# Kernel optimization log

Measured on AMD Instinct MI355X. Metric: run time of the kernel, lower is better.

## Reference

```python
import jax, jax.numpy as jnp
import numpy as np

D = 2048      # d_model
FF = 8192     # d_ff
S = 4096      # seq_len == max_len
EPS = 1.1920929e-07  # torch.finfo(float32).eps (nn.RMSNorm default when eps=None)
SCALE = float(np.sqrt(D))


def _rms_norm(x, w):
    # x: [S, D]
    return x * jax.lax.rsqrt(jnp.mean(x * x, axis=-1, keepdims=True) + EPS) * w


def _rope(x, cos, sin):
    # x: [S, D]; cos/sin: [S, D/2]
    x1, x2 = jnp.split(x, 2, axis=-1)
    return jnp.concatenate([x1 * cos - x2 * sin, x1 * sin + x2 * cos], axis=-1)


def setup_inputs() -> dict:
    key = jax.random.key(0)
    ks = jax.random.split(key, 9)

    def w(k, shape, scale=0.02):
        return jax.random.normal(k, shape, dtype=jnp.float32) * scale

    x = jax.random.normal(ks[0], (S, D), dtype=jnp.float32)
    # torch nn.Linear stores weight as [out, in]; forward is x @ W.T
    wq = w(ks[1], (D, D))
    wk = w(ks[2], (D, D))
    wv = w(ks[3], (D, D))
    wo = w(ks[4], (D, D))
    w_gate = w(ks[5], (FF, D))
    w_up = w(ks[6], (FF, D))
    w_down = w(ks[7], (D, FF))
    w_rn1 = jnp.ones((D,), dtype=jnp.float32)
    w_rn2 = jnp.ones((D,), dtype=jnp.float32)
    # RoPE caches (buffers)
    freqs = 1.0 / 10000.0 ** (jnp.arange(0, D, 2, dtype=jnp.float32) / D)
    t = jnp.arange(S, dtype=jnp.float32)
    angles = jnp.outer(t, freqs)  # [S, D/2]
    cos = jnp.cos(angles)
    sin = jnp.sin(angles)
    return dict(x=x, w_rn1=w_rn1, wq=wq, wk=wk, wv=wv, wo=wo,
                w_rn2=w_rn2, w_gate=w_gate, w_up=w_up, w_down=w_down,
                cos=cos, sin=sin)


def reference(x, w_rn1, wq, wk, wv, wo, w_rn2, w_gate, w_up, w_down, cos, sin):
    h = _rms_norm(x, w_rn1)                      # [S, D]
    q = _rope(h @ wq.T, cos, sin)                # [S, D]
    k = _rope(h @ wk.T, cos, sin)                # [S, D]
    v = h @ wv.T                                 # [S, D]
    attn = jax.nn.softmax(q @ k.T / SCALE, axis=-1)  # [S, S]
    x = x + (attn @ v) @ wo.T                    # residual 1
    h = _rms_norm(x, w_rn2)
    ffn = (jax.nn.silu(h @ w_gate.T) * (h @ w_up.T)) @ w_down.T  # SwiGLU
    return x + ffn
```

## Files before the change

### kernel.cpp

```cpp
#include <hip/hip_runtime.h>

#define S_LEN 4096
#define D_MODEL 2048
#define FF_DIM 8192
#define QKV_LD 6144

typedef __attribute__((ext_vector_type(8))) short s16x8;
typedef __attribute__((ext_vector_type(4))) short s16x4;
typedef __attribute__((ext_vector_type(4))) float f32x4;

__device__ __forceinline__ short f2bf(float f) {
  union { float f; unsigned u; } c; c.f = f;
  unsigned r = (c.u + 0x7fffu + ((c.u >> 16) & 1u)) >> 16;
  return (short)r;
}
__device__ __forceinline__ float bf2f(short s) {
  union { unsigned u; float f; } c; c.u = ((unsigned)(unsigned short)s) << 16;
  return c.f;
}

#define GLDS16(g, l) __builtin_amdgcn_global_load_lds( \
    (const __attribute__((address_space(1))) unsigned*)(g), \
    (__attribute__((address_space(3))) unsigned*)(l), 16, 0, 0)

__device__ __forceinline__ int swz(int b) {
  return b ^ (((b >> 7) & 7) << 4);
}

#define BAR()   __builtin_amdgcn_s_barrier()
#define LGKM0() asm volatile("s_waitcnt lgkmcnt(0)" ::: "memory")
#define VMC(n)  asm volatile("s_waitcnt vmcnt(" #n ")" ::: "memory")

__global__ void conv_f32_bf16(const float* __restrict__ in, short* __restrict__ out, long n) {
  long i = ((long)blockIdx.x * blockDim.x + threadIdx.x) * 8;
  if (i >= n) return;
  f32x4 a = *(const f32x4*)(in + i);
  f32x4 b = *(const f32x4*)(in + i + 4);
  s16x8 o;
  o[0] = f2bf(a[0]); o[1] = f2bf(a[1]); o[2] = f2bf(a[2]); o[3] = f2bf(a[3]);
  o[4] = f2bf(b[0]); o[5] = f2bf(b[1]); o[6] = f2bf(b[2]); o[7] = f2bf(b[3]);
  *(s16x8*)(out + i) = o;
}

__global__ void rmsnorm_kernel(const float* __restrict__ x, const float* __restrict__ w,
                               short* __restrict__ out) {
  const int row = blockIdx.x;
  const int t = threadIdx.x;
  const float* xr = x + (long)row * D_MODEL;
  f32x4 v0 = ((const f32x4*)xr)[t];
  f32x4 v1 = ((const f32x4*)xr)[256 + t];
  float ss = v0[0]*v0[0] + v0[1]*v0[1] + v0[2]*v0[2] + v0[3]*v0[3]
           + v1[0]*v1[0] + v1[1]*v1[1] + v1[2]*v1[2] + v1[3]*v1[3];
  #pragma unroll
  for (int o = 32; o > 0; o >>= 1) ss += __shfl_xor(ss, o, 64);
  __shared__ float red[4];
  if ((t & 63) == 0) red[t >> 6] = ss;
  __syncthreads();
  ss = red[0] + red[1] + red[2] + red[3];
  float scale = rsqrtf(ss * (1.0f / D_MODEL) + 1.1920929e-07f);
  f32x4 w0 = ((const f32x4*)w)[t];
  f32x4 w1 = ((const f32x4*)w)[256 + t];
  s16x4 o0, o1;
  #pragma unroll
  for (int i = 0; i < 4; i++) {
    o0[i] = f2bf(v0[i] * scale * w0[i]);
    o1[i] = f2bf(v1[i] * scale * w1[i]);
  }
  short* orow = out + (long)row * D_MODEL;
  ((s16x4*)orow)[t] = o0;
  ((s16x4*)orow)[256 + t] = o1;
}

__global__ void rope_kernel(short* __restrict__ qkv,
                            const float* __restrict__ cosb, const float* __restrict__ sinb) {
  const int s = blockIdx.x;
  short* row = qkv + (long)s * QKV_LD + (blockIdx.y ? D_MODEL : 0);
  const int j = threadIdx.x * 4;
  f32x4 c = *(const f32x4*)(cosb + (long)s * (D_MODEL / 2) + j);
  f32x4 sn = *(const f32x4*)(sinb + (long)s * (D_MODEL / 2) + j);
  s16x4 x1 = *(s16x4*)(row + j);
  s16x4 x2 = *(s16x4*)(row + (D_MODEL / 2) + j);
  s16x4 o1, o2;
  #pragma unroll
  for (int i = 0; i < 4; i++) {
    float a = bf2f(x1[i]), b = bf2f(x2[i]);
    o1[i] = f2bf(a * c[i] - b * sn[i]);
    o2[i] = f2bf(a * sn[i] + b * c[i]);
  }
  *(s16x4*)(row + j) = o1;
  *(s16x4*)(row + (D_MODEL / 2) + j) = o2;
}

__global__ void transpose_kernel(const short* __restrict__ in, short* __restrict__ out,
                                 int R, int C, int ld) {
  __shared__ short tile[32][33];
  const int bx = blockIdx.x * 32, by = blockIdx.y * 32;
  const int x = threadIdx.x, y = threadIdx.y;
  #pragma unroll
  for (int i = 0; i < 32; i += 8) tile[y + i][x] = in[(long)(by + y + i) * ld + bx + x];
  __syncthreads();
  #pragma unroll
  for (int i = 0; i < 32; i += 8) out[(long)(bx + y + i) * R + by + x] = tile[x][y + i];
}

__global__ void softmax_kernel(const float* __restrict__ sraw, short* __restrict__ pb) {
  const int row = blockIdx.x;
  const int t = threadIdx.x;
  const float* rp = sraw + (long)row * S_LEN;
  f32x4 v[4];
  #pragma unroll
  for (int i = 0; i < 4; i++) v[i] = ((const f32x4*)rp)[i * 256 + t];
  float m = -1e30f;
  #pragma unroll
  for (int i = 0; i < 4; i++)
    m = fmaxf(m, fmaxf(fmaxf(v[i][0], v[i][1]), fmaxf(v[i][2], v[i][3])));
  #pragma unroll
  for (int o = 32; o > 0; o >>= 1) m = fmaxf(m, __shfl_xor(m, o, 64));
  __shared__ float redm[4], reds[4];
  if ((t & 63) == 0) redm[t >> 6] = m;
  __syncthreads();
  m = fmaxf(fmaxf(redm[0], redm[1]), fmaxf(redm[2], redm[3]));
  float sum = 0.f;
  #pragma unroll
  for (int i = 0; i < 4; i++) {
    #pragma unroll
    for (int j = 0; j < 4; j++) { v[i][j] = __expf(v[i][j] - m); sum += v[i][j]; }
  }
  #pragma unroll
  for (int o = 32; o > 0; o >>= 1) sum += __shfl_xor(sum, o, 64);
  if ((t & 63) == 0) reds[t >> 6] = sum;
  __syncthreads();
  sum = reds[0] + reds[1] + reds[2] + reds[3];
  float inv = 1.0f / sum;
  short* prow = pb + (long)row * S_LEN;
  #pragma unroll
  for (int i = 0; i < 4; i++) {
    s16x4 o;
    #pragma unroll
    for (int j = 0; j < 4; j++) o[j] = f2bf(v[i][j] * inv);
    ((s16x4*)prow)[i * 256 + t] = o;
  }
}

template <int EPI>
__device__ __forceinline__ void epi_store(float v, long idx, float* Cf, short* Cb,
                                          const short* gmul, const float* res, float scale) {
  if (EPI == 0)      Cb[idx] = f2bf(v);
  else if (EPI == 1) Cb[idx] = f2bf(v / (1.0f + __expf(-v)));
  else if (EPI == 2) Cb[idx] = f2bf(bf2f(gmul[idx]) * v);
  else if (EPI == 3) Cf[idx] = v * scale;
  else               Cf[idx] = res[idx] + v;
}

template <int EPI>
__global__ __launch_bounds__(512)
void gemm8p_n256(const short* __restrict__ A, const short* __restrict__ B,
                 float* __restrict__ Cf, short* __restrict__ Cb,
                 const short* __restrict__ gmul, const float* __restrict__ res,
                 int K, int lda, int ldb, int ldc, float scale) {
  __shared__ short lds[2][32768];
  const int t = threadIdx.x;
  const int lane = t & 63, wid = t >> 6;
  const int wr = wid >> 2, wc = wid & 3;
  const int llo = lane & 15, lhi = lane >> 4;

  const int nwg = gridDim.x * gridDim.y;
  int bid = blockIdx.y * gridDim.x + blockIdx.x;
  bid = (bid & 7) * (nwg >> 3) + (bid >> 3);
  const long m0 = (long)(bid / gridDim.x) * 256;
  const long n0 = (long)(bid % gridDim.x) * 256;

  const int c0 = t, c1 = t + 512;
  const int sb0 = swz(c0 * 16), sb1 = swz(c1 * 16);
  const short* srcA0 = A + (m0 + (sb0 >> 7)) * (long)lda + ((sb0 & 127) >> 1);
  const short* srcA1 = A + (m0 + (sb1 >> 7)) * (long)lda + ((sb1 & 127) >> 1);
  const short* srcB0 = B + (n0 + (sb0 >> 7)) * (long)ldb + ((sb0 & 127) >> 1);
  const short* srcB1 = B + (n0 + (sb1 >> 7)) * (long)ldb + ((sb1 & 127) >> 1);
  const long dA = 128L * lda, dB = 128L * ldb;
  const int NT = K >> 6, NI = NT >> 1;

  int aof[4][2], bof[2][2];
  #pragma unroll
  for (int mf = 0; mf < 4; mf++)
    #pragma unroll
    for (int ks = 0; ks < 2; ks++)
      aof[mf][ks] = swz((wr * 128 + mf * 16 + llo) * 128 + ks * 64 + lhi * 16) >> 1;
  #pragma unroll
  for (int nf = 0; nf < 2; nf++)
    #pragma unroll
    for (int ks = 0; ks < 2; ks++)
      bof[nf][ks] = swz(32768 + (wc * 64 + nf * 16 + llo) * 128 + ks * 64 + lhi * 16) >> 1;

  f32x4 acc[8][4];
  #pragma unroll
  for (int m = 0; m < 8; m++)
    #pragma unroll
    for (int n = 0; n < 4; n++) acc[m][n] = (f32x4)(0.f);

  s16x8 ar[4][2], b0r[2][2], b1r[2][2];

  auto stage = [&](int tt, int p) {
    if (tt >= NT) return;
    short* dst = (short*)lds[tt & 1] + p * 8192;
    const long kk = (long)tt * 64;
    const short *s0, *s1;
    if (p == 0)      { s0 = srcA0;      s1 = srcA1; }
    else if (p == 1) { s0 = srcA0 + dA; s1 = srcA1 + dA; }
    else if (p == 2) { s0 = srcB0;      s1 = srcB1; }
    else             { s0 = srcB0 + dB; s1 = srcB1 + dB; }
    GLDS16(s0 + kk, dst + c0 * 8);
    GLDS16(s1 + kk, dst + c1 * 8);
  };

#define LDA6(BUF, MH) { const short* lp = (const short*)lds[BUF]; \
  _Pragma("unroll") for (int mf = 0; mf < 4; mf++) \
  _Pragma("unroll") for (int ks = 0; ks < 2; ks++) \
    ar[mf][ks] = *(const s16x8*)(lp + aof[mf][ks] + (MH) * 4096); }
#define LDB6(BUF, NH, DST) { const short* lp = (const short*)lds[BUF]; \
  _Pragma("unroll") for (int nf = 0; nf < 2; nf++) \
  _Pragma("unroll") for (int ks = 0; ks < 2; ks++) \
    DST[nf][ks] = *(const s16x8*)(lp + bof[nf][ks] + (NH) * 2048); }
#define MFMAQ6(MH, NH, BR) { __builtin_amdgcn_s_setprio(1); \
  _Pragma("unroll") for (int ks = 0; ks < 2; ks++) \
  _Pragma("unroll") for (int mf = 0; mf < 4; mf++) \
  _Pragma("unroll") for (int nf = 0; nf < 2; nf++) \
    acc[(MH)*4+mf][(NH)*2+nf] = __builtin_amdgcn_mfma_f32_16x16x32_bf16( \
        ar[mf][ks], BR[nf][ks], acc[(MH)*4+mf][(NH)*2+nf], 0, 0, 0); \
  __builtin_amdgcn_s_setprio(0); }

  stage(0, 0); stage(0, 1); stage(0, 2); stage(0, 3);
  stage(1, 2); stage(1, 3);
  VMC(4); BAR();

  for (int it = 0; it < NI; ++it) {
    const int tt = it * 2;
    const bool last = (it == NI - 1);
    LDA6(0, 0); LDB6(0, 0, b0r); stage(tt + 1, 0);
    BAR(); LGKM0(); MFMAQ6(0, 0, b0r); BAR();
    LDB6(0, 1, b1r); stage(tt + 1, 1);
    BAR(); LGKM0(); MFMAQ6(0, 1, b1r); BAR();
    LDA6(0, 1); stage(tt + 2, 2);
    BAR(); LGKM0(); MFMAQ6(1, 1, b1r); BAR();
    stage(tt + 2, 3);
    if (last) { VMC(0); } else { VMC(4); }
    BAR(); MFMAQ6(1, 0, b0r); BAR();
    LDA6(1, 0); LDB6(1, 0, b0r); stage(tt + 2, 0);
    BAR(); LGKM0(); MFMAQ6(0, 0, b0r); BAR();
    LDB6(1, 1, b1r); stage(tt + 2, 1);
    BAR(); LGKM0(); MFMAQ6(0, 1, b1r); BAR();
    LDA6(1, 1); stage(tt + 3, 2);
    BAR(); LGKM0(); MFMAQ6(1, 1, b1r); BAR();
    stage(tt + 3, 3);
    if (last) { VMC(0); } else { VMC(4); }
    BAR(); MFMAQ6(1, 0, b0r); BAR();
  }

  #pragma unroll
  for (int mf = 0; mf < 8; mf++) {
    const long row0 = m0 + wr * 128 + mf * 16 + lhi * 4;
    #pragma unroll
    for (int j = 0; j < 4; j++) {
      const long col = n0 + wc * 64 + (j >> 1) * 32 + (j & 1) * 16 + llo;
      #pragma unroll
      for (int r = 0; r < 4; r++)
        epi_store<EPI>(acc[mf][j][r], (row0 + r) * (long)ldc + col, Cf, Cb, gmul, res, scale);
    }
  }
#undef LDA6
#undef LDB6
#undef MFMAQ6
}

template <int EPI>
__global__ __launch_bounds__(512)
void gemm8p_n128(const short* __restrict__ A, const short* __restrict__ B,
                 float* __restrict__ Cf, short* __restrict__ Cb,
                 const short* __restrict__ gmul, const float* __restrict__ res,
                 int K, int lda, int ldb, int ldc, float scale) {
  __shared__ short lds[3][24576];
  const int t = threadIdx.x;
  const int lane = t & 63, wid = t >> 6;
  const int wr = wid >> 1, wc = wid & 1;
  const int llo = lane & 15, lhi = lane >> 4;

  const int nwg = gridDim.x * gridDim.y;
  int bid = blockIdx.y * gridDim.x + blockIdx.x;
  bid = (bid & 7) * (nwg >> 3) + (bid >> 3);
  const long m0 = (long)(bid / gridDim.x) * 256;
  const long n0 = (long)(bid % gridDim.x) * 128;

  const int c0 = t, c1 = t + 512;
  const int sb0 = swz(c0 * 16), sb1 = swz(c1 * 16);
  const short* srcA0 = A + (m0 + (sb0 >> 7)) * (long)lda + ((sb0 & 127) >> 1);
  const short* srcA1 = A + (m0 + (sb1 >> 7)) * (long)lda + ((sb1 & 127) >> 1);
  const short* srcB0 = B + (n0 + (sb0 >> 7)) * (long)ldb + ((sb0 & 127) >> 1);
  const short* srcB1 = B + (n0 + (sb1 >> 7)) * (long)ldb + ((sb1 & 127) >> 1);
  const long dA = 128L * lda;
  const int NT = K >> 6;

  int aof[4][2], bof[2][2];
  #pragma unroll
  for (int mf = 0; mf < 4; mf++)
    #pragma unroll
    for (int ks = 0; ks < 2; ks++)
      aof[mf][ks] = swz((wr * 64 + mf * 16 + llo) * 128 + ks * 64 + lhi * 16) >> 1;
  #pragma unroll
  for (int nf = 0; nf < 2; nf++)
    #pragma unroll
    for (int ks = 0; ks < 2; ks++)
      bof[nf][ks] = swz(32768 + (wc * 64 + nf * 16 + llo) * 128 + ks * 64 + lhi * 16) >> 1;

  f32x4 acc[4][4];
  #pragma unroll
  for (int m = 0; m < 4; m++)
    #pragma unroll
    for (int n = 0; n < 4; n++) acc[m][n] = (f32x4)(0.f);

  s16x8 ar[4][2], br[2][2];

  auto stage = [&](int tt, int slot, int p) {
    if (tt >= NT) return;
    short* dst = (short*)lds[slot] + p * 8192;
    const long kk = (long)tt * 64;
    const short *s0, *s1;
    if (p == 0)      { s0 = srcA0;      s1 = srcA1; }
    else if (p == 1) { s0 = srcA0 + dA; s1 = srcA1 + dA; }
    else             { s0 = srcB0;      s1 = srcB1; }
    GLDS16(s0 + kk, dst + c0 * 8);
    GLDS16(s1 + kk, dst + c1 * 8);
  };

#define LDA3(CUR) { const short* lp = (const short*)lds[CUR]; \
  _Pragma("unroll") for (int mf = 0; mf < 4; mf++) \
  _Pragma("unroll") for (int ks = 0; ks < 2; ks++) \
    ar[mf][ks] = *(const s16x8*)(lp + aof[mf][ks]); }
#define LDB3(CUR, NH) { const short* lp = (const short*)lds[CUR]; \
  _Pragma("unroll") for (int nf = 0; nf < 2; nf++) \
  _Pragma("unroll") for (int ks = 0; ks < 2; ks++) \
    br[nf][ks] = *(const s16x8*)(lp + bof[nf][ks] + (NH) * 2048); }
#define MFMAQ3(NH) { __builtin_amdgcn_s_setprio(1); \
  _Pragma("unroll") for (int ks = 0; ks < 2; ks++) \
  _Pragma("unroll") for (int mf = 0; mf < 4; mf++) \
  _Pragma("unroll") for (int nf = 0; nf < 2; nf++) \
    acc[mf][(NH)*2+nf] = __builtin_amdgcn_mfma_f32_16x16x32_bf16( \
        ar[mf][ks], br[nf][ks], acc[mf][(NH)*2+nf], 0, 0, 0); \
  __builtin_amdgcn_s_setprio(0); }

  stage(0, 0, 0); stage(0, 0, 1); stage(0, 0, 2);
  stage(1, 1, 0); stage(1, 1, 1); stage(1, 1, 2);
  VMC(6); BAR();

  int cur = 0;
  for (int tt = 0; tt < NT; ++tt) {
    const int s2 = (cur >= 1) ? cur - 1 : 2;
    LDA3(cur); LDB3(cur, 0); stage(tt + 2, s2, 0); stage(tt + 2, s2, 1);
    BAR(); LGKM0(); MFMAQ3(0); BAR();
    LDB3(cur, 1); stage(tt + 2, s2, 2);
    if (tt >= NT - 2) { VMC(0); } else { VMC(6); }
    BAR(); LGKM0(); MFMAQ3(1); BAR();
    cur = (cur == 2) ? 0 : cur + 1;
  }

  #pragma unroll
  for (int mf = 0; mf < 4; mf++) {
    const long row0 = m0 + wr * 64 + mf * 16 + lhi * 4;
    #pragma unroll
    for (int j = 0; j < 4; j++) {
      const long col = n0 + wc * 64 + (j >> 1) * 32 + (j & 1) * 16 + llo;
      #pragma unroll
      for (int r = 0; r < 4; r++)
        epi_store<EPI>(acc[mf][j][r], (row0 + r) * (long)ldc + col, Cf, Cb, gmul, res, scale);
    }
  }
#undef LDA3
#undef LDB3
#undef MFMAQ3
}

extern "C" void kernel_launch(void* const* d_in, const int* in_sizes, int n_in,
                              void* d_out, int out_size, void* d_ws, size_t ws_size,
                              hipStream_t stream) {
  const float* x      = (const float*)d_in[0];
  const float* w_rn1  = (const float*)d_in[1];
  const float* wq     = (const float*)d_in[2];
  const float* wk     = (const float*)d_in[3];
  const float* wv     = (const float*)d_in[4];
  const float* wo     = (const float*)d_in[5];
  const float* w_rn2  = (const float*)d_in[6];
  const float* w_gate = (const float*)d_in[7];
  const float* w_up   = (const float*)d_in[8];
  const float* w_down = (const float*)d_in[9];
  const float* cosb   = (const float*)d_in[10];
  const float* sinb   = (const float*)d_in[11];
  float* out = (float*)d_out;

  const long S = S_LEN, D = D_MODEL, FF = FF_DIM;
  char* ws = (char*)d_ws;
  size_t off = 0;
  auto alloc = [&](size_t bytes) { void* p = ws + off; off += (bytes + 255) & ~(size_t)255; return p; };

  short* qkv  = (short*)alloc(S * QKV_LD * 2);
  short* vT   = (short*)alloc(D * S * 2);
  short* hb   = (short*)alloc(S * D * 2);
  float* x1   = (float*)alloc(S * D * 4);
  short* wbuf = (short*)alloc(FF * D * 2);
  char*  u2   = (char*)alloc(S * S * 4);
  float* sraw = (float*)u2;
  short* gbuf = (short*)u2;
  short* pb   = (short*)alloc(S * S * 2);

  const float inv_scale = 1.0f / sqrtf((float)D_MODEL);
  const long DD = D * D, FD = FF * D;
  const int convDD = (int)(DD / 8 / 256), convFD = (int)(FD / 8 / 256);
  dim3 blk(256), blk5(512);
  dim3 gQKV(3 * D_MODEL / 256, S_LEN / 256);
  dim3 gS(S_LEN / 256, S_LEN / 256);
  dim3 gN2048(D_MODEL / 128, S_LEN / 256);
  dim3 gF(FF_DIM / 256, S_LEN / 256);

  rmsnorm_kernel<<<S_LEN, 256, 0, stream>>>(x, w_rn1, hb);
  conv_f32_bf16<<<convDD, blk, 0, stream>>>(wq, wbuf, DD);
  conv_f32_bf16<<<convDD, blk, 0, stream>>>(wk, wbuf + DD, DD);
  conv_f32_bf16<<<convDD, blk, 0, stream>>>(wv, wbuf + 2 * DD, DD);
  gemm8p_n256<0><<<gQKV, blk5, 0, stream>>>(hb, wbuf, nullptr, qkv, nullptr, nullptr,
                                            D_MODEL, D_MODEL, D_MODEL, QKV_LD, 1.f);
  rope_kernel<<<dim3(S_LEN, 2), blk, 0, stream>>>(qkv, cosb, sinb);
  transpose_kernel<<<dim3(D_MODEL / 32, S_LEN / 32), dim3(32, 8), 0, stream>>>(
      qkv + 2 * D_MODEL, vT, S_LEN, D_MODEL, QKV_LD);
  gemm8p_n256<3><<<gS, blk5, 0, stream>>>(qkv, qkv + D_MODEL, sraw, nullptr, nullptr, nullptr,
                                          D_MODEL, QKV_LD, QKV_LD, S_LEN, inv_scale);
  softmax_kernel<<<S_LEN, 256, 0, stream>>>(sraw, pb);
  gemm8p_n128<0><<<gN2048, blk5, 0, stream>>>(pb, vT, nullptr, qkv + 2 * D_MODEL, nullptr, nullptr,
                                              S_LEN, S_LEN, S_LEN, QKV_LD, 1.f);
  conv_f32_bf16<<<convDD, blk, 0, stream>>>(wo, wbuf, DD);
  gemm8p_n128<4><<<gN2048, blk5, 0, stream>>>(qkv + 2 * D_MODEL, wbuf, x1, nullptr, nullptr, x,
                                              D_MODEL, QKV_LD, D_MODEL, D_MODEL, 1.f);
  rmsnorm_kernel<<<S_LEN, 256, 0, stream>>>(x1, w_rn2, hb);
  conv_f32_bf16<<<convFD, blk, 0, stream>>>(w_gate, wbuf, FD);
  gemm8p_n256<1><<<gF, blk5, 0, stream>>>(hb, wbuf, nullptr, gbuf, nullptr, nullptr,
                                          D_MODEL, D_MODEL, D_MODEL, FF_DIM, 1.f);
  conv_f32_bf16<<<convFD, blk, 0, stream>>>(w_up, wbuf, FD);
  gemm8p_n256<2><<<gF, blk5, 0, stream>>>(hb, wbuf, nullptr, gbuf, gbuf, nullptr,
                                          D_MODEL, D_MODEL, D_MODEL, FF_DIM, 1.f);
  conv_f32_bf16<<<convFD, blk, 0, stream>>>(w_down, wbuf, FD);
  gemm8p_n128<4><<<gN2048, blk5, 0, stream>>>(gbuf, wbuf, out, nullptr, nullptr, x1,
                                              FF_DIM, FF_DIM, FF_DIM, D_MODEL, 1.f);
}
```

Before: 858.9 us.

## Restructure GEMM main loops to one barrier per K-tile with staged lgkmcnt waits

Both GEMM kernels drop the eight-phase, barrier-heavy ping-pong schedule. Each K-tile now issues all LDS fragment reads up front, then all global-to-LDS prefetches for a later tile. MFMA groups are gated by partial lgkmcnt waits, and a single barrier closes each iteration. This cuts barrier count and lets MFMAs start while the remaining LDS reads are still in flight. The trade-offs are more fragment registers live at once (a0r/a1r/b0r/b1r), and in the 256x256 kernel a wait for all outstanding global loads (vmcnt 0) every iteration, so prefetch can only overlap one tile of compute.

```diff
diff --git a/kernel.cpp b/kernel.cpp
--- a/kernel.cpp
+++ b/kernel.cpp
@@ -28,8 +28,9 @@
 }
 
 #define BAR()   __builtin_amdgcn_s_barrier()
-#define LGKM0() asm volatile("s_waitcnt lgkmcnt(0)" ::: "memory")
 #define VMC(n)  asm volatile("s_waitcnt vmcnt(" #n ")" ::: "memory")
+#define LGKM(n) asm volatile("s_waitcnt lgkmcnt(" #n ")" ::: "memory"); \
+                __builtin_amdgcn_sched_barrier(0)
 
 __global__ void conv_f32_bf16(const float* __restrict__ in, short* __restrict__ out, long n) {
   long i = ((long)blockIdx.x * blockDim.x + threadIdx.x) * 8;
@@ -177,7 +178,7 @@
   const short* srcB0 = B + (n0 + (sb0 >> 7)) * (long)ldb + ((sb0 & 127) >> 1);
   const short* srcB1 = B + (n0 + (sb1 >> 7)) * (long)ldb + ((sb1 & 127) >> 1);
   const long dA = 128L * lda, dB = 128L * ldb;
-  const int NT = K >> 6, NI = NT >> 1;
+  const int NT = K >> 6;
 
   int aof[4][2], bof[2][2];
   #pragma unroll
@@ -197,62 +198,52 @@
     #pragma unroll
     for (int n = 0; n < 4; n++) acc[m][n] = (f32x4)(0.f);
 
-  s16x8 ar[4][2], b0r[2][2], b1r[2][2];
-
-  auto stage = [&](int tt, int p) {
+  s16x8 a0r[4][2], a1r[4][2], b0r[2][2], b1r[2][2];
+
+  auto stageAll = [&](int tt) {
     if (tt >= NT) return;
-    short* dst = (short*)lds[tt & 1] + p * 8192;
+    short* dst = (short*)lds[tt & 1];
     const long kk = (long)tt * 64;
-    const short *s0, *s1;
-    if (p == 0)      { s0 = srcA0;      s1 = srcA1; }
-    else if (p == 1) { s0 = srcA0 + dA; s1 = srcA1 + dA; }
-    else if (p == 2) { s0 = srcB0;      s1 = srcB1; }
-    else             { s0 = srcB0 + dB; s1 = srcB1 + dB; }
-    GLDS16(s0 + kk, dst + c0 * 8);
-    GLDS16(s1 + kk, dst + c1 * 8);
+    GLDS16(srcA0 + kk,      dst + c0 * 8);
+    GLDS16(srcA1 + kk,      dst + c1 * 8);
+    GLDS16(srcA0 + dA + kk, dst + 8192 + c0 * 8);
+    GLDS16(srcA1 + dA + kk, dst + 8192 + c1 * 8);
+    GLDS16(srcB0 + kk,      dst + 16384 + c0 * 8);
+    GLDS16(srcB1 + kk,      dst + 16384 + c1 * 8);
+    GLDS16(srcB0 + dB + kk, dst + 24576 + c0 * 8);
+    GLDS16(srcB1 + dB + kk, dst + 24576 + c1 * 8);
   };
 
-#define LDA6(BUF, MH) { const short* lp = (const short*)lds[BUF]; \
+#define RDA6(DST, MH) { \
   _Pragma("unroll") for (int mf = 0; mf < 4; mf++) \
   _Pragma("unroll") for (int ks = 0; ks < 2; ks++) \
-    ar[mf][ks] = *(const s16x8*)(lp + aof[mf][ks] + (MH) * 4096); }
-#define LDB6(BUF, NH, DST) { const short* lp = (const short*)lds[BUF]; \
+    DST[mf][ks] = *(const s16x8*)(lp + aof[mf][ks] + (MH) * 4096); }
+#define RDB6(DST, NH) { \
   _Pragma("unroll") for (int nf = 0; nf < 2; nf++) \
   _Pragma("unroll") for (int ks = 0; ks < 2; ks++) \
     DST[nf][ks] = *(const s16x8*)(lp + bof[nf][ks] + (NH) * 2048); }
-#define MFMAQ6(MH, NH, BR) { __builtin_amdgcn_s_setprio(1); \
+#define MQ6(AR, BR, MH, NH) { \
   _Pragma("unroll") for (int ks = 0; ks < 2; ks++) \
   _Pragma("unroll") for (int mf = 0; mf < 4; mf++) \
   _Pragma("unroll") for (int nf = 0; nf < 2; nf++) \
     acc[(MH)*4+mf][(NH)*2+nf] = __builtin_amdgcn_mfma_f32_16x16x32_bf16( \
-        ar[mf][ks], BR[nf][ks], acc[(MH)*4+mf][(NH)*2+nf], 0, 0, 0); \
-  __builtin_amdgcn_s_setprio(0); }
-
-  stage(0, 0); stage(0, 1); stage(0, 2); stage(0, 3);
-  stage(1, 2); stage(1, 3);
-  VMC(4); BAR();
-
-  for (int it = 0; it < NI; ++it) {
-    const int tt = it * 2;
-    const bool last = (it == NI - 1);
-    LDA6(0, 0); LDB6(0, 0, b0r); stage(tt + 1, 0);
-    BAR(); LGKM0(); MFMAQ6(0, 0, b0r); BAR();
-    LDB6(0, 1, b1r); stage(tt + 1, 1);
-    BAR(); LGKM0(); MFMAQ6(0, 1, b1r); BAR();
-    LDA6(0, 1); stage(tt + 2, 2);
-    BAR(); LGKM0(); MFMAQ6(1, 1, b1r); BAR();
-    stage(tt + 2, 3);
-    if (last) { VMC(0); } else { VMC(4); }
-    BAR(); MFMAQ6(1, 0, b0r); BAR();
-    LDA6(1, 0); LDB6(1, 0, b0r); stage(tt + 2, 0);
-    BAR(); LGKM0(); MFMAQ6(0, 0, b0r); BAR();
-    LDB6(1, 1, b1r); stage(tt + 2, 1);
-    BAR(); LGKM0(); MFMAQ6(0, 1, b1r); BAR();
-    LDA6(1, 1); stage(tt + 3, 2);
-    BAR(); LGKM0(); MFMAQ6(1, 1, b1r); BAR();
-    stage(tt + 3, 3);
-    if (last) { VMC(0); } else { VMC(4); }
-    BAR(); MFMAQ6(1, 0, b0r); BAR();
+        AR[mf][ks], BR[nf][ks], acc[(MH)*4+mf][(NH)*2+nf], 0, 0, 0); }
+
+  stageAll(0);
+  VMC(0); BAR();
+  for (int tt = 0; tt < NT; ++tt) {
+    const short* lp = (const short*)lds[tt & 1];
+    RDA6(a0r, 0); RDB6(b0r, 0); RDB6(b1r, 1); RDA6(a1r, 1);
+    stageAll(tt + 1);
+    LGKM(12);
+    __builtin_amdgcn_s_setprio(1); MQ6(a0r, b0r, 0, 0); __builtin_amdgcn_s_setprio(0);
+    LGKM(8);
+    __builtin_amdgcn_s_setprio(1); MQ6(a0r, b1r, 0, 1); __builtin_amdgcn_s_setprio(0);
+    LGKM(0);
+    __builtin_amdgcn_s_setprio(1); MQ6(a1r, b1r, 1, 1); MQ6(a1r, b0r, 1, 0);
+    __builtin_amdgcn_s_setprio(0);
+    VMC(0);
+    BAR();
   }
 
   #pragma unroll
@@ -266,9 +257,9 @@
         epi_store<EPI>(acc[mf][j][r], (row0 + r) * (long)ldc + col, Cf, Cb, gmul, res, scale);
     }
   }
-#undef LDA6
-#undef LDB6
-#undef MFMAQ6
+#undef RDA6
+#undef RDB6
+#undef MQ6
 }
 
 template <int EPI>
@@ -316,48 +307,49 @@
     #pragma unroll
     for (int n = 0; n < 4; n++) acc[m][n] = (f32x4)(0.f);
 
-  s16x8 ar[4][2], br[2][2];
-
-  auto stage = [&](int tt, int slot, int p) {
+  s16x8 ar[4][2], b0r[2][2], b1r[2][2];
+
+  auto stageAll = [&](int tt, int slot) {
     if (tt >= NT) return;
-    short* dst = (short*)lds[slot] + p * 8192;
+    short* dst = (short*)lds[slot];
     const long kk = (long)tt * 64;
-    const short *s0, *s1;
-    if (p == 0)      { s0 = srcA0;      s1 = srcA1; }
-    else if (p == 1) { s0 = srcA0 + dA; s1 = srcA1 + dA; }
-    else             { s0 = srcB0;      s1 = srcB1; }
-    GLDS16(s0 + kk, dst + c0 * 8);
-    GLDS16(s1 + kk, dst + c1 * 8);
+    GLDS16(srcA0 + kk,      dst + c0 * 8);
+    GLDS16(srcA1 + kk,      dst + c1 * 8);
+    GLDS16(srcA0 + dA + kk, dst + 8192 + c0 * 8);
+    GLDS16(srcA1 + dA + kk, dst + 8192 + c1 * 8);
+    GLDS16(srcB0 + kk,      dst + 16384 + c0 * 8);
+    GLDS16(srcB1 + kk,      dst + 16384 + c1 * 8);
   };
 
-#define LDA3(CUR) { const short* lp = (const short*)lds[CUR]; \
+#define RDA3() { \
   _Pragma("unroll") for (int mf = 0; mf < 4; mf++) \
   _Pragma("unroll") for (int ks = 0; ks < 2; ks++) \
     ar[mf][ks] = *(const s16x8*)(lp + aof[mf][ks]); }
-#define LDB3(CUR, NH) { const short* lp = (const short*)lds[CUR]; \
+#define RDB3(DST, NH) { \
   _Pragma("unroll") for (int nf = 0; nf < 2; nf++) \
   _Pragma("unroll") for (int ks = 0; ks < 2; ks++) \
-    br[nf][ks] = *(const s16x8*)(lp + bof[nf][ks] + (NH) * 2048); }
-#define MFMAQ3(NH) { __builtin_amdgcn_s_setprio(1); \
+    DST[nf][ks] = *(const s16x8*)(lp + bof[nf][ks] + (NH) * 2048); }
+#define MQ3(BR, NH) { \
   _Pragma("unroll") for (int ks = 0; ks < 2; ks++) \
   _Pragma("unroll") for (int mf = 0; mf < 4; mf++) \
   _Pragma("unroll") for (int nf = 0; nf < 2; nf++) \
     acc[mf][(NH)*2+nf] = __builtin_amdgcn_mfma_f32_16x16x32_bf16( \
-        ar[mf][ks], br[nf][ks], acc[mf][(NH)*2+nf], 0, 0, 0); \
-  __builtin_amdgcn_s_setprio(0); }
-
-  stage(0, 0, 0); stage(0, 0, 1); stage(0, 0, 2);
-  stage(1, 1, 0); stage(1, 1, 1); stage(1, 1, 2);
+        ar[mf][ks], BR[nf][ks], acc[mf][(NH)*2+nf], 0, 0, 0); }
+
+  stageAll(0, 0); stageAll(1, 1);
   VMC(6); BAR();
-
   int cur = 0;
   for (int tt = 0; tt < NT; ++tt) {
+    const short* lp = (const short*)lds[cur];
+    RDA3(); RDB3(b0r, 0); RDB3(b1r, 1);
     const int s2 = (cur >= 1) ? cur - 1 : 2;
-    LDA3(cur); LDB3(cur, 0); stage(tt + 2, s2, 0); stage(tt + 2, s2, 1);
-    BAR(); LGKM0(); MFMAQ3(0); BAR();
-    LDB3(cur, 1); stage(tt + 2, s2, 2);
+    stageAll(tt + 2, s2);
+    LGKM(4);
+    __builtin_amdgcn_s_setprio(1); MQ3(b0r, 0); __builtin_amdgcn_s_setprio(0);
+    LGKM(0);
+    __builtin_amdgcn_s_setprio(1); MQ3(b1r, 1); __builtin_amdgcn_s_setprio(0);
     if (tt >= NT - 2) { VMC(0); } else { VMC(6); }
-    BAR(); LGKM0(); MFMAQ3(1); BAR();
+    BAR();
     cur = (cur == 2) ? 0 : cur + 1;
   }
 
@@ -372,9 +364,9 @@
         epi_store<EPI>(acc[mf][j][r], (row0 + r) * (long)ldc + col, Cf, Cb, gmul, res, scale);
     }
   }
-#undef LDA3
-#undef LDB3
-#undef MFMAQ3
+#undef RDA3
+#undef RDB3
+#undef MQ3
 }
 
 extern "C" void kernel_launch(void* const* d_in, const int* in_sizes, int n_in,
```

After: 977.0 us. +13.7%, slower.

## Fuse gate and up FFN GEMMs into one dual-accumulator SwiGLU kernel

Applied to the files above, without the earlier changes.

Adds a gemm_ffn kernel that stages one A tile and both gate and up weight tiles per K step. It keeps two accumulator sets and applies silu(g)*u in the epilogue, so the separate gate and up GEMMs and the bf16 gate buffer write and re-read go away, and the A tiles are loaded once instead of twice. The up weights are converted into the spare pb buffer. The QKV GEMM also moves to the 256x128 tile kernel to launch more workgroups. The fused kernel uses a simpler double-buffered loop with a full VMC(0) wait every iteration and carries two accumulator sets, which can cost latency hiding and occupancy.

```diff
diff --git a/kernel.cpp b/kernel.cpp
--- a/kernel.cpp
+++ b/kernel.cpp
@@ -144,10 +144,8 @@
 
 template <int EPI>
 __device__ __forceinline__ void epi_store(float v, long idx, float* Cf, short* Cb,
-                                          const short* gmul, const float* res, float scale) {
+                                          const float* res, float scale) {
   if (EPI == 0)      Cb[idx] = f2bf(v);
-  else if (EPI == 1) Cb[idx] = f2bf(v / (1.0f + __expf(-v)));
-  else if (EPI == 2) Cb[idx] = f2bf(bf2f(gmul[idx]) * v);
   else if (EPI == 3) Cf[idx] = v * scale;
   else               Cf[idx] = res[idx] + v;
 }
@@ -156,7 +154,7 @@
 __global__ __launch_bounds__(512)
 void gemm8p_n256(const short* __restrict__ A, const short* __restrict__ B,
                  float* __restrict__ Cf, short* __restrict__ Cb,
-                 const short* __restrict__ gmul, const float* __restrict__ res,
+                 const float* __restrict__ res,
                  int K, int lda, int ldb, int ldc, float scale) {
   __shared__ short lds[2][32768];
   const int t = threadIdx.x;
@@ -263,7 +261,7 @@
       const long col = n0 + wc * 64 + (j >> 1) * 32 + (j & 1) * 16 + llo;
       #pragma unroll
       for (int r = 0; r < 4; r++)
-        epi_store<EPI>(acc[mf][j][r], (row0 + r) * (long)ldc + col, Cf, Cb, gmul, res, scale);
+        epi_store<EPI>(acc[mf][j][r], (row0 + r) * (long)ldc + col, Cf, Cb, res, scale);
     }
   }
 #undef LDA6
@@ -275,7 +273,7 @@
 __global__ __launch_bounds__(512)
 void gemm8p_n128(const short* __restrict__ A, const short* __restrict__ B,
                  float* __restrict__ Cf, short* __restrict__ Cb,
-                 const short* __restrict__ gmul, const float* __restrict__ res,
+                 const float* __restrict__ res,
                  int K, int lda, int ldb, int ldc, float scale) {
   __shared__ short lds[3][24576];
   const int t = threadIdx.x;
@@ -369,12 +367,128 @@
       const long col = n0 + wc * 64 + (j >> 1) * 32 + (j & 1) * 16 + llo;
       #pragma unroll
       for (int r = 0; r < 4; r++)
-        epi_store<EPI>(acc[mf][j][r], (row0 + r) * (long)ldc + col, Cf, Cb, gmul, res, scale);
+        epi_store<EPI>(acc[mf][j][r], (row0 + r) * (long)ldc + col, Cf, Cb, res, scale);
     }
   }
 #undef LDA3
 #undef LDB3
 #undef MFMAQ3
+}
+
+__global__ __launch_bounds__(512)
+void gemm_ffn(const short* __restrict__ A, const short* __restrict__ Bg,
+              const short* __restrict__ Bu, short* __restrict__ Cb,
+              int K, int lda, int ldb, int ldc) {
+  __shared__ short lds[2][32768];
+  const int t = threadIdx.x;
+  const int lane = t & 63, wid = t >> 6;
+  const int wr = wid >> 1, wc = wid & 1;
+  const int llo = lane & 15, lhi = lane >> 4;
+
+  const int nwg = gridDim.x * gridDim.y;
+  int bid = blockIdx.y * gridDim.x + blockIdx.x;
+  bid = (bid & 7) * (nwg >> 3) + (bid >> 3);
+  const long m0 = (long)(bid / gridDim.x) * 256;
+  const long n0 = (long)(bid % gridDim.x) * 128;
+
+  const short* sA[4];
+  #pragma unroll
+  for (int j = 0; j < 4; j++) {
+    int sb = swz((t + j * 512) * 16);
+    sA[j] = A + (m0 + (sb >> 7)) * (long)lda + ((sb & 127) >> 1);
+  }
+  const short *sG[2], *sU[2];
+  #pragma unroll
+  for (int j = 0; j < 2; j++) {
+    int sbg = swz((t + 2048 + j * 512) * 16) - 32768;
+    sG[j] = Bg + (n0 + (sbg >> 7)) * (long)ldb + ((sbg & 127) >> 1);
+    int sbu = swz((t + 3072 + j * 512) * 16) - 49152;
+    sU[j] = Bu + (n0 + (sbu >> 7)) * (long)ldb + ((sbu & 127) >> 1);
+  }
+  const int NT = K >> 6;
+
+  int aof[4][2], bofg[2][2], bofu[2][2];
+  #pragma unroll
+  for (int mf = 0; mf < 4; mf++)
+    #pragma unroll
+    for (int ks = 0; ks < 2; ks++)
+      aof[mf][ks] = swz((wr * 64 + mf * 16 + llo) * 128 + ks * 64 + lhi * 16) >> 1;
+  #pragma unroll
+  for (int nf = 0; nf < 2; nf++)
+    #pragma unroll
+    for (int ks = 0; ks < 2; ks++) {
+      bofg[nf][ks] = swz(32768 + (wc * 64 + nf * 16 + llo) * 128 + ks * 64 + lhi * 16) >> 1;
+      bofu[nf][ks] = swz(49152 + (wc * 64 + nf * 16 + llo) * 128 + ks * 64 + lhi * 16) >> 1;
+    }
+
+  f32x4 accg[4][4], accu[4][4];
+  #pragma unroll
+  for (int m = 0; m < 4; m++)
+    #pragma unroll
+    for (int n = 0; n < 4; n++) { accg[m][n] = (f32x4)(0.f); accu[m][n] = (f32x4)(0.f); }
+
+  s16x8 ar[4][2], br[2][2];
+
+  auto stageAll = [&](int tt) {
+    if (tt >= NT) return;
+    short* dst = (short*)lds[tt & 1];
+    const long kk = (long)tt * 64;
+    #pragma unroll
+    for (int j = 0; j < 4; j++) GLDS16(sA[j] + kk, dst + (t + j * 512) * 8);
+    #pragma unroll
+    for (int j = 0; j < 2; j++) GLDS16(sG[j] + kk, dst + (t + 2048 + j * 512) * 8);
+    #pragma unroll
+    for (int j = 0; j < 2; j++) GLDS16(sU[j] + kk, dst + (t + 3072 + j * 512) * 8);
+  };
+
+#define FLDA(CUR) { const short* lp = (const short*)lds[CUR]; \
+  _Pragma("unroll") for (int mf = 0; mf < 4; mf++) \
+  _Pragma("unroll") for (int ks = 0; ks < 2; ks++) \
+    ar[mf][ks] = *(const s16x8*)(lp + aof[mf][ks]); }
+#define FLDB(CUR, TBL, NH) { const short* lp = (const short*)lds[CUR]; \
+  _Pragma("unroll") for (int nf = 0; nf < 2; nf++) \
+  _Pragma("unroll") for (int ks = 0; ks < 2; ks++) \
+    br[nf][ks] = *(const s16x8*)(lp + TBL[nf][ks] + (NH) * 2048); }
+#define FMQ(ACC, NH) { __builtin_amdgcn_s_setprio(1); \
+  _Pragma("unroll") for (int ks = 0; ks < 2; ks++) \
+  _Pragma("unroll") for (int mf = 0; mf < 4; mf++) \
+  _Pragma("unroll") for (int nf = 0; nf < 2; nf++) \
+    ACC[mf][(NH)*2+nf] = __builtin_amdgcn_mfma_f32_16x16x32_bf16( \
+        ar[mf][ks], br[nf][ks], ACC[mf][(NH)*2+nf], 0, 0, 0); \
+  __builtin_amdgcn_s_setprio(0); }
+
+  stageAll(0);
+  VMC(0); BAR();
+  for (int tt = 0; tt < NT; ++tt) {
+    const int cur = tt & 1;
+    FLDA(cur); FLDB(cur, bofg, 0); stageAll(tt + 1);
+    BAR(); LGKM0(); FMQ(accg, 0); BAR();
+    FLDB(cur, bofg, 1);
+    BAR(); LGKM0(); FMQ(accg, 1); BAR();
+    FLDB(cur, bofu, 0);
+    BAR(); LGKM0(); FMQ(accu, 0); BAR();
+    FLDB(cur, bofu, 1);
+    BAR(); LGKM0(); FMQ(accu, 1);
+    VMC(0); BAR();
+  }
+
+  #pragma unroll
+  for (int mf = 0; mf < 4; mf++) {
+    const long row0 = m0 + wr * 64 + mf * 16 + lhi * 4;
+    #pragma unroll
+    for (int j = 0; j < 4; j++) {
+      const long col = n0 + wc * 64 + (j >> 1) * 32 + (j & 1) * 16 + llo;
+      #pragma unroll
+      for (int r = 0; r < 4; r++) {
+        float g = accg[mf][j][r], u = accu[mf][j][r];
+        float v = (g / (1.0f + __expf(-g))) * u;
+        Cb[(row0 + r) * (long)ldc + col] = f2bf(v);
+      }
+    }
+  }
+#undef FLDA
+#undef FLDB
+#undef FMQ
 }
 
 extern "C" void kernel_launch(void* const* d_in, const int* in_sizes, int n_in,
@@ -413,36 +527,33 @@
   const long DD = D * D, FD = FF * D;
   const int convDD = (int)(DD / 8 / 256), convFD = (int)(FD / 8 / 256);
   dim3 blk(256), blk5(512);
-  dim3 gQKV(3 * D_MODEL / 256, S_LEN / 256);
+  dim3 gQKV(3 * D_MODEL / 128, S_LEN / 256);
   dim3 gS(S_LEN / 256, S_LEN / 256);
   dim3 gN2048(D_MODEL / 128, S_LEN / 256);
-  dim3 gF(FF_DIM / 256, S_LEN / 256);
+  dim3 gFFN(FF_DIM / 128, S_LEN / 256);
 
   rmsnorm_kernel<<<S_LEN, 256, 0, stream>>>(x, w_rn1, hb);
   conv_f32_bf16<<<convDD, blk, 0, stream>>>(wq, wbuf, DD);
   conv_f32_bf16<<<convDD, blk, 0, stream>>>(wk, wbuf + DD, DD);
   conv_f32_bf16<<<convDD, blk, 0, stream>>>(wv, wbuf + 2 * DD, DD);
-  gemm8p_n256<0><<<gQKV, blk5, 0, stream>>>(hb, wbuf, nullptr, qkv, nullptr, nullptr,
+  gemm8p_n128<0><<<gQKV, blk5, 0, stream>>>(hb, wbuf, nullptr, qkv, nullptr,
                                             D_MODEL, D_MODEL, D_MODEL, QKV_LD, 1.f);
   rope_kernel<<<dim3(S_LEN, 2), blk, 0, stream>>>(qkv, cosb, sinb);
   transpose_kernel<<<dim3(D_MODEL / 32, S_LEN / 32), dim3(32, 8), 0, stream>>>(
       qkv + 2 * D_MODEL, vT, S_LEN, D_MODEL, QKV_LD);
-  gemm8p_n256<3><<<gS, blk5, 0, stream>>>(qkv, qkv + D_MODEL, sraw, nullptr, nullptr, nullptr,
+  gemm8p_n256<3><<<gS, blk5, 0, stream>>>(qkv, qkv + D_MODEL, sraw, nullptr, nullptr,
                                           D_MODEL, QKV_LD, QKV_LD, S_LEN, inv_scale);
   softmax_kernel<<<S_LEN, 256, 0, stream>>>(sraw, pb);
-  gemm8p_n128<0><<<gN2048, blk5, 0, stream>>>(pb, vT, nullptr, qkv + 2 * D_MODEL, nullptr, nullptr,
+  gemm8p_n128<0><<<gN2048, blk5, 0, stream>>>(pb, vT, nullptr, qkv + 2 * D_MODEL, nullptr,
                                               S_LEN, S_LEN, S_LEN, QKV_LD, 1.f);
   conv_f32_bf16<<<convDD, blk, 0, stream>>>(wo, wbuf, DD);
-  gemm8p_n128<4><<<gN2048, blk5, 0, stream>>>(qkv + 2 * D_MODEL, wbuf, x1, nullptr, nullptr, x,
+  gemm8p_n128<4><<<gN2048, blk5, 0, stream>>>(qkv + 2 * D_MODEL, wbuf, x1, nullptr, x,
                                               D_MODEL, QKV_LD, D_MODEL, D_MODEL, 1.f);
   rmsnorm_kernel<<<S_LEN, 256, 0, stream>>>(x1, w_rn2, hb);
   conv_f32_bf16<<<convFD, blk, 0, stream>>>(w_gate, wbuf, FD);
-  gemm8p_n256<1><<<gF, blk5, 0, stream>>>(hb, wbuf, nullptr, gbuf, nullptr, nullptr,
-                                          D_MODEL, D_MODEL, D_MODEL, FF_DIM, 1.f);
-  conv_f32_bf16<<<convFD, blk, 0, stream>>>(w_up, wbuf, FD);
-  gemm8p_n256<2><<<gF, blk5, 0, stream>>>(hb, wbuf, nullptr, gbuf, gbuf, nullptr,
-                                          D_MODEL, D_MODEL, D_MODEL, FF_DIM, 1.f);
+  conv_f32_bf16<<<convFD, blk, 0, stream>>>(w_up, pb, FD);
+  gemm_ffn<<<gFFN, blk5, 0, stream>>>(hb, wbuf, pb, gbuf, D_MODEL, D_MODEL, D_MODEL, FF_DIM);
   conv_f32_bf16<<<convFD, blk, 0, stream>>>(w_down, wbuf, FD);
-  gemm8p_n128<4><<<gN2048, blk5, 0, stream>>>(gbuf, wbuf, out, nullptr, nullptr, x1,
+  gemm8p_n128<4><<<gN2048, blk5, 0, stream>>>(gbuf, wbuf, out, nullptr, x1,
                                               FF_DIM, FF_DIM, FF_DIM, D_MODEL, 1.f);
 }
```

Result: no change. 861.9 us, median of 2 (+0.4%).
